# Kernel optimization log

Measured on AMD Instinct MI355X. Metric: run time of the kernel, lower is better.

Reference implementation:

```python
import jax, jax.numpy as jnp
import numpy as np

H, HKV, D, RD = 16, 2, 256, 64   # q heads, kv heads, head dim, rope dim
THETA = 10000.0


def _rope_tables(S, dtype=jnp.float32):
    inv_freq = 1.0 / (THETA ** (jnp.arange(0, RD, 2, dtype=jnp.float32) / RD))
    t = jnp.arange(S, dtype=jnp.float32)
    freqs = jnp.outer(t, inv_freq)                      # [S, RD/2]
    emb = jnp.concatenate([freqs, freqs], axis=-1)      # [S, RD]
    return jnp.cos(emb).astype(dtype), jnp.sin(emb).astype(dtype)


def _apply_rope(x, cos, sin):
    # x: [B, h, S, D]; rotate first RD dims, pass the rest through.
    xr, xp = x[..., :RD], x[..., RD:]
    half = RD // 2
    rot = jnp.concatenate([-xr[..., half:], xr[..., :half]], axis=-1)
    return jnp.concatenate([xr * cos + rot * sin, xp], axis=-1)


def setup_inputs() -> dict:
    key = jax.random.key(0)
    ks = jax.random.split(key, 6)
    B, S, E = 2, 2048, 2048
    s = 0.02
    return {
        "hidden_states": jax.random.normal(ks[0], (B, S, E), jnp.float32),
        "Wq": jax.random.normal(ks[1], (E, H * D), jnp.float32) * s,
        "Wk": jax.random.normal(ks[2], (E, HKV * D), jnp.float32) * s,
        "Wv": jax.random.normal(ks[3], (E, HKV * D), jnp.float32) * s,
        "Wg": jax.random.normal(ks[4], (E, H * D), jnp.float32) * s,
        "Wo": jax.random.normal(ks[5], (H * D, E), jnp.float32) * s,
    }


def reference(hidden_states, Wq, Wk, Wv, Wg, Wo):
    B, S, E = hidden_states.shape
    G = H // HKV  # GQA factor (8)

    q = (hidden_states @ Wq).reshape(B, S, H, D).transpose(0, 2, 1, 3)      # [B,H,S,D]
    k = (hidden_states @ Wk).reshape(B, S, HKV, D).transpose(0, 2, 1, 3)    # [B,HKV,S,D]
    v = (hidden_states @ Wv).reshape(B, S, HKV, D).transpose(0, 2, 1, 3)
    gate = jax.nn.sigmoid(hidden_states @ Wg).reshape(B, S, H, D).transpose(0, 2, 1, 3)

    cos, sin = _rope_tables(S, hidden_states.dtype)
    q = _apply_rope(q, cos, sin)
    k = _apply_rope(k, cos, sin)

    # GQA without materializing repeated KV: group query heads per KV head.
    qg = q.reshape(B, HKV, G, S, D)
    scale = D ** -0.5
    scores = jnp.einsum('bkgqd,bksd->bkgqs', qg, k) * scale                 # [B,HKV,G,S,S]
    causal = jnp.tril(jnp.ones((S, S), dtype=bool))
    neg = jnp.asarray(jnp.finfo(scores.dtype).min, scores.dtype)
    scores = jnp.where(causal, scores, neg)
    probs = jax.nn.softmax(scores, axis=-1)
    attn = jnp.einsum('bkgqs,bksd->bkgqd', probs, v).reshape(B, H, S, D)

    attn = attn * gate                                                       # output gating
    attn = attn.transpose(0, 2, 1, 3).reshape(B, S, H * D)
    return attn @ Wo
```

## Files before the change

### kernel.cpp

```cpp
#include <hip/hip_runtime.h>
#include <hip/hip_bf16.h>
#include <cstdint>

typedef __attribute__((ext_vector_type(8))) short bf16x8;
typedef __attribute__((ext_vector_type(4))) float f32x4;
typedef __attribute__((ext_vector_type(16))) float f32x16;

#define H_   16
#define HKV_ 2
#define DD   256
#define BB   2
#define SS   2048
#define EE   2048
#define MTOK (BB*SS)
#define HD   (H_*DD)

static __device__ __forceinline__ unsigned short f2bf(float f) {
  union { float f; unsigned u; } v; v.f = f;
  unsigned r = v.u + 0x7fffu + ((v.u >> 16) & 1u);
  return (unsigned short)(r >> 16);
}
static __device__ __forceinline__ float bf2f(unsigned short h) {
  union { unsigned u; float f; } v; v.u = ((unsigned)h) << 16;
  return v.f;
}

static __device__ __forceinline__ void gll16(const unsigned short* g, unsigned short* l) {
  __builtin_amdgcn_global_load_lds(
      (const __attribute__((address_space(1))) unsigned int*)g,
      (__attribute__((address_space(3))) unsigned int*)l, 16, 0, 0);
}

__global__ __launch_bounds__(256) void ga_cvt(const float* __restrict__ in,
                                              unsigned short* __restrict__ out, int n) {
  int i = (blockIdx.x * 256 + threadIdx.x) * 4;
  if (i >= n) return;
  float4 v = *(const float4*)(in + i);
  ushort4 o;
  o.x = f2bf(v.x); o.y = f2bf(v.y); o.z = f2bf(v.z); o.w = f2bf(v.w);
  *(ushort4*)(out + i) = o;
}

__global__ __launch_bounds__(256) void ga_transpose_wo(const float* __restrict__ in,
                                                       unsigned short* __restrict__ out,
                                                       int R, int C) {
  __shared__ float tile[64][65];
  int c0 = blockIdx.x * 64, r0 = blockIdx.y * 64;
  int tid = threadIdx.x;
#pragma unroll
  for (int it = 0; it < 16; ++it) {
    int idx = it * 256 + tid; int rr = idx >> 6, cc = idx & 63;
    tile[rr][cc] = in[(size_t)(r0 + rr) * C + c0 + cc];
  }
  __syncthreads();
#pragma unroll
  for (int it = 0; it < 16; ++it) {
    int idx = it * 256 + tid; int rr = idx >> 6, cc = idx & 63;
    out[(size_t)(c0 + rr) * R + r0 + cc] = f2bf(tile[cc][rr]);
  }
}

__global__ __launch_bounds__(256) void ga_pack_qkvg(const float* __restrict__ Wq,
                                                    const float* __restrict__ Wk,
                                                    const float* __restrict__ Wv,
                                                    const float* __restrict__ Wg,
                                                    unsigned short* __restrict__ out) {
  __shared__ float tile[64][65];
  int n0 = blockIdx.x * 64, k0 = blockIdx.y * 64;
  const float* src; int C, cbase;
  if (n0 < 4096)      { src = Wq; C = 4096; cbase = n0; }
  else if (n0 < 4608) { src = Wk; C = 512;  cbase = n0 - 4096; }
  else if (n0 < 5120) { src = Wv; C = 512;  cbase = n0 - 4608; }
  else                { src = Wg; C = 4096; cbase = n0 - 5120; }
  int tid = threadIdx.x;
#pragma unroll
  for (int it = 0; it < 16; ++it) {
    int idx = it * 256 + tid; int rr = idx >> 6, cc = idx & 63;
    tile[rr][cc] = src[(size_t)(k0 + rr) * C + cbase + cc];
  }
  __syncthreads();
#pragma unroll
  for (int it = 0; it < 16; ++it) {
    int idx = it * 256 + tid; int rr = idx >> 6, cc = idx & 63;
    out[(size_t)(n0 + rr) * EE + k0 + cc] = f2bf(tile[cc][rr]);
  }
}

template<int KDIM>
static __device__ __forceinline__ void gemm_loop(const unsigned short* __restrict__ A,
                                                 const unsigned short* __restrict__ Bt,
                                                 unsigned short* As, unsigned short* Bs,
                                                 int m0, int n0, f32x4 acc[4][4]) {
  int tid = threadIdx.x, lane = tid & 63, wid = tid >> 6;
  int wr = wid >> 1, wc = wid & 1;
  for (int k0 = 0; k0 < KDIM; k0 += 32) {
    __syncthreads();
#pragma unroll
    for (int r2 = 0; r2 < 2; ++r2) {
      int c = r2 * 256 + wid * 64 + lane;
      int row = c >> 2, cb = c & 3;
      gll16(A  + (size_t)(m0 + row) * KDIM + k0 + cb * 8, As + (r2 * 256 + wid * 64) * 8);
      gll16(Bt + (size_t)(n0 + row) * KDIM + k0 + cb * 8, Bs + (r2 * 256 + wid * 64) * 8);
    }
    __syncthreads();
    bf16x8 af[4], bfv[4];
#pragma unroll
    for (int mf = 0; mf < 4; ++mf)
      af[mf] = *(const bf16x8*)&As[(wr * 64 + mf * 16 + (lane & 15)) * 32 + (lane >> 4) * 8];
#pragma unroll
    for (int nf = 0; nf < 4; ++nf)
      bfv[nf] = *(const bf16x8*)&Bs[(wc * 64 + nf * 16 + (lane & 15)) * 32 + (lane >> 4) * 8];
#pragma unroll
    for (int mf = 0; mf < 4; ++mf)
#pragma unroll
      for (int nf = 0; nf < 4; ++nf)
        acc[mf][nf] = __builtin_amdgcn_mfma_f32_16x16x32_bf16(af[mf], bfv[nf], acc[mf][nf], 0, 0, 0);
  }
}

__global__ __launch_bounds__(256) void ga_gemm_qkvg(const unsigned short* __restrict__ A,
                                                    const unsigned short* __restrict__ Bt,
                                                    unsigned short* __restrict__ qo,
                                                    unsigned short* __restrict__ ko,
                                                    unsigned short* __restrict__ vo,
                                                    unsigned short* __restrict__ go) {
  __shared__ unsigned short As[128 * 32];
  __shared__ unsigned short Bs[128 * 32];
  int tid = threadIdx.x, lane = tid & 63, wid = tid >> 6;
  int wr = wid >> 1, wc = wid & 1;
  int lin = blockIdx.x;
  int xcd = lin & 7, j = lin >> 3;
  int n0 = (xcd * 9 + (j % 9)) * 128;
  int m0 = (j / 9) * 128;
  f32x4 acc[4][4];
  f32x4 z = {0.f, 0.f, 0.f, 0.f};
#pragma unroll
  for (int i = 0; i < 4; ++i)
#pragma unroll
    for (int jj = 0; jj < 4; ++jj) acc[i][jj] = z;

  gemm_loop<EE>(A, Bt, As, Bs, m0, n0, acc);

  int li = lane & 15, lg = lane >> 4;
  int nb = n0 + wc * 64;
  int mb = m0 + wr * 64;
  bool isq = nb < 4096;
  bool isk = (nb >= 4096) && (nb < 4608);
  bool isv = (nb >= 4608) && (nb < 5120);
  float invf0 = expf((float)li * -0.2878231366242601f);
  float invf1 = expf((float)(16 + li) * -0.2878231366242601f);

#pragma unroll
  for (int mf = 0; mf < 4; ++mf) {
#pragma unroll
    for (int r = 0; r < 4; ++r) {
      int m = mb + mf * 16 + lg * 4 + r;
      int bb = m >> 11, s = m & 2047;
      if (isv) {
        int hk = (nb - 4608) >> 8, hdb = (nb - 4608) & 255;
        unsigned short* dst = vo + ((size_t)(bb * HKV_ + hk) * DD + hdb) * SS + s;
#pragma unroll
        for (int nf = 0; nf < 4; ++nf)
          dst[(size_t)(nf * 16 + li) * SS] = f2bf(acc[mf][nf][r]);
      } else if (!isq && !isk) {
        int h = (nb - 5120) >> 8, hdb = (nb - 5120) & 255;
        unsigned short* dst = go + ((size_t)(bb * H_ + h) * SS + s) * DD + hdb;
#pragma unroll
        for (int nf = 0; nf < 4; ++nf) {
          float x = acc[mf][nf][r];
          dst[nf * 16 + li] = f2bf(1.f / (1.f + __expf(-x)));
        }
      } else {
        int hdb; unsigned short* dst;
        if (isq) { int h = nb >> 8; hdb = nb & 255;
                   dst = qo + ((size_t)(bb * H_ + h) * SS + s) * DD; }
        else     { int hk = (nb - 4096) >> 8; hdb = (nb - 4096) & 255;
                   dst = ko + ((size_t)(bb * HKV_ + hk) * SS + s) * DD; }
        if (hdb == 0) {
#pragma unroll
          for (int nf = 0; nf < 2; ++nf) {
            int fi = nf * 16 + li;
            float ang = (float)s * (nf ? invf1 : invf0);
            float sn, cs;
            sincosf(ang, &sn, &cs);
            float x1 = acc[mf][nf][r], x2 = acc[mf][nf + 2][r];
            dst[fi]      = f2bf(x1 * cs - x2 * sn);
            dst[fi + 32] = f2bf(x2 * cs + x1 * sn);
          }
        } else {
#pragma unroll
          for (int nf = 0; nf < 4; ++nf) dst[hdb + nf * 16 + li] = f2bf(acc[mf][nf][r]);
        }
      }
    }
  }
}

__global__ __launch_bounds__(256) void ga_gemm_out(const unsigned short* __restrict__ A,
                                                   const unsigned short* __restrict__ Bt,
                                                   float* __restrict__ C) {
  __shared__ unsigned short As[128 * 32];
  __shared__ unsigned short Bs[128 * 32];
  int tid = threadIdx.x, lane = tid & 63, wid = tid >> 6;
  int wr = wid >> 1, wc = wid & 1;
  int lin = blockIdx.x;
  int xcd = lin & 7, j = lin >> 3;
  int m0 = (xcd * 4 + (j & 3)) * 128;
  int n0 = (j >> 2) * 128;
  f32x4 acc[4][4];
  f32x4 z = {0.f, 0.f, 0.f, 0.f};
#pragma unroll
  for (int i = 0; i < 4; ++i)
#pragma unroll
    for (int jj = 0; jj < 4; ++jj) acc[i][jj] = z;

  gemm_loop<HD>(A, Bt, As, Bs, m0, n0, acc);

  int li = lane & 15, lg = lane >> 4;
#pragma unroll
  for (int mf = 0; mf < 4; ++mf)
#pragma unroll
    for (int r = 0; r < 4; ++r) {
      int m = m0 + wr * 64 + mf * 16 + lg * 4 + r;
#pragma unroll
      for (int nf = 0; nf < 4; ++nf) {
        int n = n0 + wc * 64 + nf * 16 + li;
        C[(size_t)m * EE + n] = acc[mf][nf][r];
      }
    }
}

__global__ __launch_bounds__(256) void ga_attn(const unsigned short* __restrict__ qb_,
                                               const unsigned short* __restrict__ kb,
                                               const unsigned short* __restrict__ vt,
                                               const unsigned short* __restrict__ gb,
                                               unsigned short* __restrict__ ob) {
  __shared__ unsigned short Ks[2][8192];
  __shared__ unsigned short Vs[2][8192];
  __shared__ float Xch[4][32];
  int tid = threadIdx.x, lane = tid & 63, wid = tid >> 6;
  int col = lane & 31, hi = lane >> 5;
  int L = blockIdx.x;
  int bh = L & 31, ii = L >> 5;
  int qblk = (ii < 8) ? (15 - 2 * ii) : (2 * (ii - 8));
  int q0 = qblk * 128;
  int b = bh >> 4, h = bh & 15, hk = h >> 3;
  const unsigned short* qp  = qb_ + ((size_t)(b * H_ + h) * SS) * DD;
  const unsigned short* kp  = kb + ((size_t)(b * HKV_ + hk) * SS) * DD;
  const unsigned short* vtp = vt + ((size_t)(b * HKV_ + hk) * DD) * SS;
  const unsigned short* gp  = gb + ((size_t)(b * H_ + h) * SS) * DD;

  int kgo[4], vgo[4], lob[4];
#pragma unroll
  for (int it = 0; it < 4; ++it) {
    int c = it * 256 + tid;
    int kr = c >> 5, c16 = c & 31;
    kgo[it] = kr * DD + ((c16 ^ (kr & 7)) << 3);
    int vd = c >> 2;
    int cmg = (c & 3) ^ (vd & 3);
    vgo[it] = vd * SS + (cmg << 3);
    lob[it] = (it * 256 + wid * 64) * 8;
  }

  int qwave = q0 + wid * 32;
  bf16x8 qf[16];
#pragma unroll
  for (int ks = 0; ks < 16; ++ks)
    qf[ks] = *(const bf16x8*)(qp + (size_t)(qwave + col) * DD + ks * 16 + hi * 8);

  f32x16 acc[8];
#pragma unroll
  for (int d8 = 0; d8 < 8; ++d8)
#pragma unroll
    for (int r = 0; r < 16; ++r) acc[d8][r] = 0.f;
  float mrun = -1e30f, lrun = 0.f;

  int nt = q0 / 32 + 4;
  int vs0 = ((hi) ^ (col & 3)) << 3;
  int vs1 = ((2 + hi) ^ (col & 3)) << 3;

#pragma unroll
  for (int it = 0; it < 4; ++it) {
    gll16(kp + kgo[it], &Ks[0][lob[it]]);
    gll16(vtp + vgo[it], &Vs[0][lob[it]]);
  }
  asm volatile("s_waitcnt vmcnt(0)" ::: "memory");
  __builtin_amdgcn_s_barrier();

  for (int t = 0; t < nt; ++t) {
    int kv0 = t * 32;
    int cur = t & 1;
    bool pre = (t + 1 < nt);
    if (pre) {
      int kvn = kv0 + 32;
#pragma unroll
      for (int it = 0; it < 4; ++it) {
        gll16(kp + (size_t)kvn * DD + kgo[it], &Ks[cur ^ 1][lob[it]]);
        gll16(vtp + kvn + vgo[it],             &Vs[cur ^ 1][lob[it]]);
      }
    }
    if (kv0 <= qwave + 31) {
      f32x16 sc;
#pragma unroll
      for (int r = 0; r < 16; ++r) sc[r] = 0.f;
      const unsigned short* kbase = &Ks[cur][col * 256];
      __builtin_amdgcn_s_setprio(1);
#pragma unroll
      for (int ks = 0; ks < 16; ++ks) {
        bf16x8 kfr = *(const bf16x8*)(kbase + (((ks * 2 + hi) ^ (col & 7)) << 3));
        sc = __builtin_amdgcn_mfma_f32_32x32x16_bf16(kfr, qf[ks], sc, 0, 0, 0);
      }
      __builtin_amdgcn_s_setprio(0);
      bool needmask = (kv0 + 31 > qwave);
#pragma unroll
      for (int r = 0; r < 16; ++r) {
        int kvg = kv0 + (r & 3) + 8 * (r >> 2) + 4 * hi;
        float v = sc[r] * 0.0625f;
        if (needmask && kvg > qwave + col) v = -1e30f;
        sc[r] = v;
      }
      float pm = fmaxf(sc[0], sc[1]);
#pragma unroll
      for (int r = 2; r < 16; ++r) pm = fmaxf(pm, sc[r]);
      pm = fmaxf(pm, __shfl_xor(pm, 32));
      if (!__all(pm - mrun <= 8.f)) {
        float nm = fmaxf(mrun, pm);
        float scl = __expf(mrun - nm);
        mrun = nm;
        lrun *= scl;
        if (lane < 32) Xch[wid][lane] = scl;
#pragma unroll
        for (int r = 0; r < 16; ++r) {
          float s2 = Xch[wid][(r & 3) + 8 * (r >> 2) + 4 * hi];
#pragma unroll
          for (int d8 = 0; d8 < 8; ++d8) acc[d8][r] *= s2;
        }
      }
      float rs = 0.f;
#pragma unroll
      for (int r = 0; r < 16; ++r) { float e = __expf(sc[r] - mrun); sc[r] = e; rs += e; }
      rs += __shfl_xor(rs, 32);
      lrun += rs;
      unsigned w[8];
#pragma unroll
      for (int jj = 0; jj < 8; ++jj)
        w[jj] = ((unsigned)f2bf(sc[2 * jj + 1]) << 16) | (unsigned)f2bf(sc[2 * jj]);
      unsigned x0 = (unsigned)__shfl_xor((int)w[2], 32);
      unsigned x1 = (unsigned)__shfl_xor((int)w[3], 32);
      unsigned x2 = (unsigned)__shfl_xor((int)w[0], 32);
      unsigned x3 = (unsigned)__shfl_xor((int)w[1], 32);
      unsigned x4 = (unsigned)__shfl_xor((int)w[6], 32);
      unsigned x5 = (unsigned)__shfl_xor((int)w[7], 32);
      unsigned x6 = (unsigned)__shfl_xor((int)w[4], 32);
      unsigned x7 = (unsigned)__shfl_xor((int)w[5], 32);
      union { unsigned u[4]; bf16x8 v; } pa0, pa1;
      pa0.u[0] = hi ? x0 : w[0];
      pa0.u[1] = hi ? x1 : w[1];
      pa0.u[2] = hi ? w[2] : x2;
      pa0.u[3] = hi ? w[3] : x3;
      pa1.u[0] = hi ? x4 : w[4];
      pa1.u[1] = hi ? x5 : w[5];
      pa1.u[2] = hi ? w[6] : x6;
      pa1.u[3] = hi ? w[7] : x7;
      const unsigned short* vb = &Vs[cur][0];
      __builtin_amdgcn_s_setprio(1);
#pragma unroll
      for (int d8 = 0; d8 < 8; ++d8) {
        int rb = (d8 * 32 + col) * 32;
        bf16x8 bv0 = *(const bf16x8*)(vb + rb + vs0);
        bf16x8 bv1 = *(const bf16x8*)(vb + rb + vs1);
        acc[d8] = __builtin_amdgcn_mfma_f32_32x32x16_bf16(pa0.v, bv0, acc[d8], 0, 0, 0);
        acc[d8] = __builtin_amdgcn_mfma_f32_32x32x16_bf16(pa1.v, bv1, acc[d8], 0, 0, 0);
      }
      __builtin_amdgcn_s_setprio(0);
    }
    if (pre) {
      asm volatile("s_waitcnt vmcnt(0)" ::: "memory");
    }
    __builtin_amdgcn_sched_barrier(0);
    __builtin_amdgcn_s_barrier();
  }
  if (lane < 32) Xch[wid][lane] = 1.f / lrun;
#pragma unroll
  for (int r = 0; r < 16; ++r) {
    int crow = (r & 3) + 8 * (r >> 2) + 4 * hi;
    float inv2 = Xch[wid][crow];
    int qrow = qwave + crow;
    const unsigned short* gr = gp + (size_t)qrow * DD;
    unsigned short* orow = ob + ((size_t)(b * SS + qrow)) * HD + h * DD;
#pragma unroll
    for (int d8 = 0; d8 < 8; ++d8) {
      int d = d8 * 32 + col;
      float gv = bf2f(gr[d]);
      orow[d] = f2bf(acc[d8][r] * inv2 * gv);
    }
  }
}

extern "C" void kernel_launch(void* const* d_in, const int* in_sizes, int n_in,
                              void* d_out, int out_size, void* d_ws, size_t ws_size,
                              hipStream_t stream) {
  (void)in_sizes; (void)n_in; (void)out_size;
  const float* hs = (const float*)d_in[0];
  const float* Wq = (const float*)d_in[1];
  const float* Wk = (const float*)d_in[2];
  const float* Wv = (const float*)d_in[3];
  const float* Wg = (const float*)d_in[4];
  const float* Wo = (const float*)d_in[5];
  float* out = (float*)d_out;

  const size_t off_X    = 0;
  const size_t off_Wcat = off_X    + 16777216;
  const size_t off_Wot  = off_Wcat + 37748736;
  const size_t off_q    = off_Wot  + 16777216;
  const size_t off_k    = off_q    + 33554432;
  const size_t off_v    = off_k    + 4194304;
  const size_t off_g    = off_v    + 4194304;
  const size_t off_attn = off_g    + 33554432;
  const size_t need     = off_attn + 33554432;
  if (ws_size < need) return;

  char* ws = (char*)d_ws;
  unsigned short* Xbf   = (unsigned short*)(ws + off_X);
  unsigned short* Wcat  = (unsigned short*)(ws + off_Wcat);
  unsigned short* Wot   = (unsigned short*)(ws + off_Wot);
  unsigned short* qbf   = (unsigned short*)(ws + off_q);
  unsigned short* kbf   = (unsigned short*)(ws + off_k);
  unsigned short* vbf   = (unsigned short*)(ws + off_v);
  unsigned short* gbf   = (unsigned short*)(ws + off_g);
  unsigned short* attnb = (unsigned short*)(ws + off_attn);

  ga_cvt<<<8192, 256, 0, stream>>>(hs, Xbf, MTOK * EE);
  ga_pack_qkvg<<<dim3(144, 32), 256, 0, stream>>>(Wq, Wk, Wv, Wg, Wcat);
  ga_transpose_wo<<<dim3(32, 64), 256, 0, stream>>>(Wo, Wot, HD, EE);
  ga_gemm_qkvg<<<dim3(2304), 256, 0, stream>>>(Xbf, Wcat, qbf, kbf, vbf, gbf);
  ga_attn<<<dim3(512), 256, 0, stream>>>(qbf, kbf, vbf, gbf, attnb);
  ga_gemm_out<<<dim3(512), 256, 0, stream>>>(attnb, Wot, out);
}
```

Before: 626.7 us.

## Double-buffer LDS tiles in GEMM loop to overlap global loads with MFMA

Turns the shared GEMM main loop into a two-stage LDS ping-pong. The next K-slice is fetched with direct-to-LDS loads while MFMAs run on the current slice. This replaces the two barriers per iteration with one wait plus barrier at the end, aiming to hide global memory latency in the QKVG projection and output projection GEMMs. LDS use per block doubles, which may lower occupancy.

```diff
diff --git a/kernel.cpp b/kernel.cpp
--- a/kernel.cpp
+++ b/kernel.cpp
@@ -93,28 +93,56 @@
                                                  int m0, int n0, f32x4 acc[4][4]) {
   int tid = threadIdx.x, lane = tid & 63, wid = tid >> 6;
   int wr = wid >> 1, wc = wid & 1;
-  for (int k0 = 0; k0 < KDIM; k0 += 32) {
-    __syncthreads();
-#pragma unroll
-    for (int r2 = 0; r2 < 2; ++r2) {
-      int c = r2 * 256 + wid * 64 + lane;
-      int row = c >> 2, cb = c & 3;
-      gll16(A  + (size_t)(m0 + row) * KDIM + k0 + cb * 8, As + (r2 * 256 + wid * 64) * 8);
-      gll16(Bt + (size_t)(n0 + row) * KDIM + k0 + cb * 8, Bs + (r2 * 256 + wid * 64) * 8);
-    }
-    __syncthreads();
+  int li = lane & 15, lg = lane >> 4;
+  int rowA[2], cb8[2], ldso[2];
+#pragma unroll
+  for (int r2 = 0; r2 < 2; ++r2) {
+    int c = r2 * 256 + wid * 64 + lane;
+    rowA[r2] = c >> 2;
+    cb8[r2] = (c & 3) * 8;
+    ldso[r2] = (r2 * 256 + wid * 64) * 8;
+  }
+#pragma unroll
+  for (int r2 = 0; r2 < 2; ++r2) {
+    gll16(A  + (size_t)(m0 + rowA[r2]) * KDIM + cb8[r2], As + ldso[r2]);
+    gll16(Bt + (size_t)(n0 + rowA[r2]) * KDIM + cb8[r2], Bs + ldso[r2]);
+  }
+  asm volatile("s_waitcnt vmcnt(0)" ::: "memory");
+  __builtin_amdgcn_s_barrier();
+
+  const int NK = KDIM / 32;
+  for (int t = 0; t < NK; ++t) {
+    int cur = t & 1;
+    unsigned short* Asc = As + cur * 4096;
+    unsigned short* Bsc = Bs + cur * 4096;
+    bool pre = (t + 1 < NK);
+    if (pre) {
+      int k0 = (t + 1) * 32;
+      unsigned short* Asn = As + (cur ^ 1) * 4096;
+      unsigned short* Bsn = Bs + (cur ^ 1) * 4096;
+#pragma unroll
+      for (int r2 = 0; r2 < 2; ++r2) {
+        gll16(A  + (size_t)(m0 + rowA[r2]) * KDIM + k0 + cb8[r2], Asn + ldso[r2]);
+        gll16(Bt + (size_t)(n0 + rowA[r2]) * KDIM + k0 + cb8[r2], Bsn + ldso[r2]);
+      }
+    }
     bf16x8 af[4], bfv[4];
 #pragma unroll
     for (int mf = 0; mf < 4; ++mf)
-      af[mf] = *(const bf16x8*)&As[(wr * 64 + mf * 16 + (lane & 15)) * 32 + (lane >> 4) * 8];
+      af[mf] = *(const bf16x8*)&Asc[(wr * 64 + mf * 16 + li) * 32 + lg * 8];
 #pragma unroll
     for (int nf = 0; nf < 4; ++nf)
-      bfv[nf] = *(const bf16x8*)&Bs[(wc * 64 + nf * 16 + (lane & 15)) * 32 + (lane >> 4) * 8];
+      bfv[nf] = *(const bf16x8*)&Bsc[(wc * 64 + nf * 16 + li) * 32 + lg * 8];
 #pragma unroll
     for (int mf = 0; mf < 4; ++mf)
 #pragma unroll
       for (int nf = 0; nf < 4; ++nf)
         acc[mf][nf] = __builtin_amdgcn_mfma_f32_16x16x32_bf16(af[mf], bfv[nf], acc[mf][nf], 0, 0, 0);
+    if (pre) {
+      asm volatile("s_waitcnt vmcnt(0)" ::: "memory");
+    }
+    __builtin_amdgcn_sched_barrier(0);
+    __builtin_amdgcn_s_barrier();
   }
 }
 
@@ -124,8 +152,8 @@
                                                     unsigned short* __restrict__ ko,
                                                     unsigned short* __restrict__ vo,
                                                     unsigned short* __restrict__ go) {
-  __shared__ unsigned short As[128 * 32];
-  __shared__ unsigned short Bs[128 * 32];
+  __shared__ unsigned short As[2 * 128 * 32];
+  __shared__ unsigned short Bs[2 * 128 * 32];
   int tid = threadIdx.x, lane = tid & 63, wid = tid >> 6;
   int wr = wid >> 1, wc = wid & 1;
   int lin = blockIdx.x;
@@ -199,8 +227,8 @@
 __global__ __launch_bounds__(256) void ga_gemm_out(const unsigned short* __restrict__ A,
                                                    const unsigned short* __restrict__ Bt,
                                                    float* __restrict__ C) {
-  __shared__ unsigned short As[128 * 32];
-  __shared__ unsigned short Bs[128 * 32];
+  __shared__ unsigned short As[2 * 128 * 32];
+  __shared__ unsigned short Bs[2 * 128 * 32];
   int tid = threadIdx.x, lane = tid & 63, wid = tid >> 6;
   int wr = wid >> 1, wc = wid & 1;
   int lin = blockIdx.x;
```

After: 621.1 us. No clear change (-0.9%).
